# Kernel optimization log

Measured on AMD Instinct MI355X. Metric: run time of the kernel, lower is better.

## Reference

```python
import jax, jax.numpy as jnp
import numpy as np

B, L, H, C, A = 8, 4096, 512, 64, 512
NEG = -1000000000.0

def setup_inputs() -> dict:
    key = jax.random.key(0)
    ks = jax.random.split(key, 6)
    hidden_states = jax.random.normal(ks[0], (B, L, H), dtype=jnp.float32)
    critical_mask = jax.random.randint(ks[1], (B, L, 1), 0, 2).astype(bool)
    count_active_channels = jax.random.randint(ks[2], (B, L, 1), 0, 64).astype(jnp.int32)
    channel_activity = jax.random.normal(ks[3], (B, L, C), dtype=jnp.float32)
    proj_w = jax.random.normal(ks[4], (H, A), dtype=jnp.float32) * 0.02
    proj_b = jnp.zeros((A,), dtype=jnp.float32)
    score_w = jax.random.normal(ks[5], (A, 1), dtype=jnp.float32) * 0.02
    score_b = jnp.zeros((1,), dtype=jnp.float32)
    return {"hidden_states": hidden_states, "critical_mask": critical_mask,
            "count_active_channels": count_active_channels,
            "channel_activity": channel_activity,
            "proj_w": proj_w, "proj_b": proj_b,
            "score_w": score_w, "score_b": score_b}

def reference(hidden_states, critical_mask, count_active_channels, channel_activity,
              proj_w, proj_b, score_w, score_b):
    mask = critical_mask[..., 0].astype(bool)                       # (B,L)
    count_signal = count_active_channels[..., 0].astype(hidden_states.dtype)  # (B,L)
    activity = jnp.maximum(channel_activity.astype(hidden_states.dtype), 0.0)  # (B,L,C)
    # score(tanh(proj(h)))  -> (B,L)
    logits = (jnp.tanh(hidden_states @ proj_w + proj_b) @ score_w + score_b)[..., 0]
    logits = logits + jnp.log1p(jnp.maximum(count_signal, 0.0))
    channel_mask = activity > 0                                      # (B,L,C)
    # (B,C,L) masked logits with log1p activity bias
    channel_logits = logits[:, None, :] + jnp.log1p(jnp.swapaxes(activity, 1, 2))
    channel_logits = jnp.where(jnp.swapaxes(channel_mask, 1, 2), channel_logits, NEG)
    has_channel_any = channel_mask.any(axis=1)                       # (B,C)
    weights = jax.nn.softmax(channel_logits, axis=-1)                # (B,C,L)
    weights = jnp.where(has_channel_any[..., None], weights, 0.0)
    channel_contexts = jnp.einsum('bcl,blh->bch', weights, hidden_states)  # (B,C,H)
    fallback = jnp.broadcast_to(hidden_states[:, -1:, :], channel_contexts.shape)
    channel_contexts = jnp.where(has_channel_any[..., None], channel_contexts, fallback)
    mix = activity / jnp.maximum(activity.sum(axis=2, keepdims=True), 1.0)  # (B,L,C)
    expanded_context = jnp.einsum('blc,bch->blh', mix, channel_contexts)    # (B,L,H)
    max_count = jnp.maximum(count_signal.max(axis=1, keepdims=True), 1.0)
    density_gate = 1.0 + count_signal / max_count                    # (B,L)
    attended = jnp.where(mask[..., None], expanded_context * density_gate[..., None], hidden_states)
    return attended, weights
```

## Files before the change

kernel.cpp:

```cpp
#include <hip/hip_runtime.h>
#include <hip/hip_bf16.h>
#include <math.h>

#define NEGV (-1000000000.0f)
constexpr int Bb = 8, Ll = 4096, Hh = 512, Cc = 64, Aa = 512;

typedef float f32x4 __attribute__((ext_vector_type(4)));
typedef short s16x8 __attribute__((ext_vector_type(8)));

__device__ inline ushort f2bf(float f) {
  union { float f; uint u; } v; v.f = f;
  uint u = v.u;
  return (ushort)((u + 0x7FFFu + ((u >> 16) & 1u)) >> 16);
}

__device__ inline uint bfpack2(float x, float y) {
  __hip_bfloat162 h = __float22bfloat162_rn(make_float2(x, y));
  union { __hip_bfloat162 h; uint u; } v; v.h = h;
  return v.u;
}

__device__ __forceinline__ void gl16(const void* g, void* l) {
  __builtin_amdgcn_global_load_lds(
      reinterpret_cast<const __attribute__((address_space(1))) unsigned int*>(
          reinterpret_cast<uintptr_t>(g)),
      reinterpret_cast<__attribute__((address_space(3))) unsigned int*>(
          reinterpret_cast<uintptr_t>(l)),
      16, 0, 0);
}

__global__ void k_cvt(const float* __restrict__ hid, ushort* __restrict__ hidb) {
  size_t i = (size_t)blockIdx.x * 256 + threadIdx.x;
#pragma unroll
  for (int r = 0; r < 4; ++r, i += 524288) {
    const float4* p = (const float4*)(hid + i * 8);
    float4 x = p[0], y = p[1];
    uint4 u = {bfpack2(x.x, x.y), bfpack2(x.z, x.w),
               bfpack2(y.x, y.y), bfpack2(y.z, y.w)};
    *(uint4*)(hidb + i * 8) = u;
  }
}

__global__ void k_init(const int* __restrict__ cnt, const float* __restrict__ sb,
                       float* __restrict__ logits, int* __restrict__ cmax) {
  int i = blockIdx.x * 256 + threadIdx.x;
  int c = cnt[i];
  logits[i] = sb[0] + log1pf(fmaxf((float)c, 0.f));
  int m = c;
#pragma unroll
  for (int s = 32; s; s >>= 1) m = max(m, __shfl_xor(m, s));
  if ((threadIdx.x & 63) == 0) atomicMax(&cmax[i >> 12], m);
}

__global__ void kT_pw(const float* __restrict__ pw, ushort* __restrict__ pwT) {
  __shared__ ushort s[64][65];
  const int k0 = (blockIdx.x >> 3) * 64, a0 = (blockIdx.x & 7) * 64;
  const int t = threadIdx.x;
#pragma unroll
  for (int i = 0; i < 16; ++i) {
    int e = t + i * 256;
    int kk = e >> 6, aa = e & 63;
    s[aa][kk] = f2bf(pw[(size_t)(k0 + kk) * Aa + a0 + aa]);
  }
  __syncthreads();
#pragma unroll
  for (int i = 0; i < 16; ++i) {
    int e = t + i * 256;
    int aa = e >> 6, kk = e & 63;
    pwT[(size_t)(a0 + aa) * Hh + k0 + kk] = s[aa][kk];
  }
}

__global__ __launch_bounds__(256) void k0_gemm(
    const ushort* __restrict__ hidb, const ushort* __restrict__ pwT,
    const float* __restrict__ pb, const float* __restrict__ sw,
    float* __restrict__ logits) {
  __shared__ ushort smem[16384];
  const int bm = blockIdx.x, bn = blockIdx.y;
  const int tid = threadIdx.x;
  const int lane = tid & 63;
  const int w = tid >> 6;
  const int wm = w >> 1, wn = w & 1;
  const int lc = lane & 15, lq = lane >> 4;

  const int srow = tid >> 2;
  const int schunk = (tid & 3) * 8;
  const ushort* Ag = hidb + ((size_t)(bm * 128 + srow)) * Hh + schunk;
  const ushort* Bg = pwT + ((size_t)(bn * 128 + srow)) * Hh + schunk;
  const int wrow = 16 * w;

  f32x4 acc[4][4];
#pragma unroll
  for (int mi = 0; mi < 4; ++mi)
#pragma unroll
    for (int ni = 0; ni < 4; ++ni) acc[mi][ni] = (f32x4){0.f, 0.f, 0.f, 0.f};

  const int aoffc = (wm * 64 + lc) * 32 + lq * 8;
  const int boffc = (wn * 64 + lc) * 32 + lq * 8;

#define K0_STAGE(buf, kb)                                   \
  do {                                                      \
    const ushort* ag = Ag + (kb) * 32;                      \
    const ushort* bg = Bg + (kb) * 32;                      \
    ushort* la = smem + (buf) * 4096 + wrow * 32;           \
    ushort* lb = smem + 8192 + (buf) * 4096 + wrow * 32;    \
    gl16(ag, la);                                           \
    gl16(ag + 64 * Hh, la + 64 * 32);                       \
    gl16(bg, lb);                                           \
    gl16(bg + 64 * Hh, lb + 64 * 32);                       \
  } while (0)

  K0_STAGE(0, 0);
  __syncthreads();

  int buf = 0;
  for (int kb = 0; kb < 16; ++kb) {
    if (kb < 15) K0_STAGE(buf ^ 1, kb + 1);
    const ushort* Ab = smem + buf * 4096;
    const ushort* Bt = smem + 8192 + buf * 4096;
    s16x8 af[4], bfr[4];
#pragma unroll
    for (int mi = 0; mi < 4; ++mi)
      af[mi] = *(const s16x8*)(Ab + aoffc + mi * 512);
#pragma unroll
    for (int ni = 0; ni < 4; ++ni)
      bfr[ni] = *(const s16x8*)(Bt + boffc + ni * 512);
#pragma unroll
    for (int mi = 0; mi < 4; ++mi)
#pragma unroll
      for (int ni = 0; ni < 4; ++ni)
        acc[mi][ni] = __builtin_amdgcn_mfma_f32_16x16x32_bf16(
            af[mi], bfr[ni], acc[mi][ni], 0, 0, 0);
    __syncthreads();
    buf ^= 1;
  }
#undef K0_STAGE

  float pbv[4], swv[4];
#pragma unroll
  for (int ni = 0; ni < 4; ++ni) {
    int n = bn * 128 + wn * 64 + ni * 16 + lc;
    pbv[ni] = pb[n];
    swv[ni] = sw[n];
  }
#pragma unroll
  for (int mi = 0; mi < 4; ++mi) {
#pragma unroll
    for (int r = 0; r < 4; ++r) {
      float s = 0.f;
#pragma unroll
      for (int ni = 0; ni < 4; ++ni) {
        float x = acc[mi][ni][r] + pbv[ni];
        float e = __expf(2.f * x);
        float th = 1.f - 2.f / (e + 1.f);
        s = fmaf(th, swv[ni], s);
      }
      s += __shfl_xor(s, 1);
      s += __shfl_xor(s, 2);
      s += __shfl_xor(s, 4);
      s += __shfl_xor(s, 8);
      if (lc == 0) {
        int m = bm * 128 + wm * 64 + mi * 16 + lq * 4 + r;
        atomicAdd(&logits[m], s);
      }
    }
  }
}

__global__ void k2_transpose(const float* __restrict__ act,
                             float* __restrict__ actT,
                             float* __restrict__ dinv) {
  __shared__ float t64[64][65];
  const int b = blockIdx.x >> 6;
  const int l0 = (blockIdx.x & 63) * 64;
  const int tid = threadIdx.x;
#pragma unroll
  for (int i = 0; i < 16; ++i) {
    int e = tid + i * 256;
    int l = e >> 6, c = e & 63;
    float v = act[((size_t)(b * Ll + l0 + l)) * Cc + c];
    t64[l][c] = fmaxf(v, 0.f);
  }
  __syncthreads();
  if (tid < 64) {
    float s = 0.f;
#pragma unroll 8
    for (int c = 0; c < 64; ++c) s += t64[tid][c];
    dinv[b * Ll + l0 + tid] = 1.0f / fmaxf(s, 1.0f);
  }
#pragma unroll
  for (int i = 0; i < 16; ++i) {
    int e = tid + i * 256;
    int c = e >> 6, lq = e & 63;
    actT[((size_t)(b * Cc + c)) * Ll + l0 + lq] = t64[lq][c];
  }
}

__global__ void k3_softmax(const float* __restrict__ actT,
                           const float* __restrict__ logits,
                           float* __restrict__ wout,
                           ushort* __restrict__ wb16,
                           int* __restrict__ hasany) {
  __shared__ float rmax[4], rcnt[4], rsum[4];
  const int bid = blockIdx.x;
  const int b = bid >> 6;
  const int tid = threadIdx.x;
  const float* arow = actT + (size_t)bid * Ll;

  float xs[16];
  float lmax = NEGV, fcnt = 0.f;
#pragma unroll
  for (int i = 0; i < 16; ++i) {
    int l = tid + i * 256;
    float a = arow[l];
    float x;
    if (a > 0.f) {
      x = logits[b * Ll + l] + log1pf(a);
      fcnt += 1.f;
    } else {
      x = NEGV;
    }
    xs[i] = x;
    lmax = fmaxf(lmax, x);
  }
#pragma unroll
  for (int m = 32; m >= 1; m >>= 1) {
    lmax = fmaxf(lmax, __shfl_xor(lmax, m));
    fcnt += __shfl_xor(fcnt, m);
  }
  if ((tid & 63) == 0) { rmax[tid >> 6] = lmax; rcnt[tid >> 6] = fcnt; }
  __syncthreads();
  float m4 = fmaxf(fmaxf(rmax[0], rmax[1]), fmaxf(rmax[2], rmax[3]));
  float call = rcnt[0] + rcnt[1] + rcnt[2] + rcnt[3];

  float lsum = 0.f;
#pragma unroll
  for (int i = 0; i < 16; ++i) {
    float e = expf(xs[i] - m4);
    xs[i] = e;
    lsum += e;
  }
#pragma unroll
  for (int m = 32; m >= 1; m >>= 1) lsum += __shfl_xor(lsum, m);
  if ((tid & 63) == 0) rsum[tid >> 6] = lsum;
  __syncthreads();
  float s = rsum[0] + rsum[1] + rsum[2] + rsum[3];
  int any = call > 0.5f;
  float inv = any ? 1.0f / s : 0.f;
#pragma unroll
  for (int i = 0; i < 16; ++i) {
    float wv = xs[i] * inv;
    wout[(size_t)bid * Ll + tid + i * 256] = wv;
    wb16[(size_t)bid * Ll + tid + i * 256] = f2bf(wv);
  }
  if (tid == 0) hasany[bid] = any;
}

__global__ __launch_bounds__(256) void k5_mfma(
    const ushort* __restrict__ wb16, const ushort* __restrict__ hidb,
    float* __restrict__ pbuf) {
  const int b = blockIdx.x, nt = blockIdx.y, kz = blockIdx.z;
  const int tid = threadIdx.x;
  const int w = tid >> 6, lane = tid & 63;
  const int lc = lane & 15, lq = lane >> 4;
  const int h0 = nt * 128 + w * 32;

  f32x4 acc[4][2];
#pragma unroll
  for (int mi = 0; mi < 4; ++mi)
#pragma unroll
    for (int ni = 0; ni < 2; ++ni) acc[mi][ni] = (f32x4){0.f, 0.f, 0.f, 0.f};

  const ushort* Abase =
      wb16 + (size_t)b * Cc * Ll + (size_t)lc * Ll + kz * 256 + lq * 8;
  const ushort* Bbase =
      hidb + ((size_t)(b * Ll + kz * 256 + lq * 8)) * Hh + h0 + lc;

  for (int kb = 0; kb < 8; ++kb) {
    s16x8 af[4];
#pragma unroll
    for (int mi = 0; mi < 4; ++mi)
      af[mi] = *(const s16x8*)(Abase + (size_t)mi * 16 * Ll + kb * 32);
    s16x8 bfv[2];
#pragma unroll
    for (int ni = 0; ni < 2; ++ni) {
      const ushort* bp = Bbase + (size_t)kb * 32 * Hh + ni * 16;
      s16x8 t;
#pragma unroll
      for (int j = 0; j < 8; ++j) t[j] = (short)bp[(size_t)j * Hh];
      bfv[ni] = t;
    }
#pragma unroll
    for (int mi = 0; mi < 4; ++mi)
#pragma unroll
      for (int ni = 0; ni < 2; ++ni)
        acc[mi][ni] = __builtin_amdgcn_mfma_f32_16x16x32_bf16(
            af[mi], bfv[ni], acc[mi][ni], 0, 0, 0);
  }

  const size_t obase = ((size_t)(kz * Bb + b)) * Cc * Hh;
#pragma unroll
  for (int mi = 0; mi < 4; ++mi)
#pragma unroll
    for (int ni = 0; ni < 2; ++ni)
#pragma unroll
      for (int r = 0; r < 4; ++r)
        pbuf[obase + (size_t)(mi * 16 + lq * 4 + r) * Hh + h0 + ni * 16 + lc] =
            acc[mi][ni][r];
}

__global__ void k6_reduce(const float* __restrict__ pbuf,
                          const int* __restrict__ hasany,
                          const float* __restrict__ hid,
                          float* __restrict__ cctx) {
  int idx = blockIdx.x * 256 + threadIdx.x;
  float s = 0.f;
#pragma unroll
  for (int z = 0; z < 16; ++z) s += pbuf[(size_t)z * 262144 + idx];
  int bc = idx >> 9, b = idx >> 15, h = idx & 511;
  cctx[idx] = hasany[bc] ? s : hid[((size_t)(b * Ll + Ll - 1)) * Hh + h];
}

__global__ __launch_bounds__(256) void k7_out(
    const float* __restrict__ hid, const float* __restrict__ act,
    const float* __restrict__ dinv, const float* __restrict__ cctx,
    const int* __restrict__ mask, const int* __restrict__ cnt,
    const int* __restrict__ cmax, float* __restrict__ out) {
  __shared__ float cct[64][128];
  __shared__ float mixs[64][64];
  __shared__ float gateb[64];
  __shared__ int maskb[64];
  const int b = blockIdx.x;
  const int l0 = blockIdx.y * 64;
  const int h0 = blockIdx.z * 128;
  const int tid = threadIdx.x;
  const int w = tid >> 6;

  {
    const float* g = cctx + (size_t)(b * Cc + (tid >> 5)) * Hh + h0 + (tid & 31) * 4;
    float* lb = &cct[0][0] + (2 * w) * 128;
#pragma unroll
    for (int i = 0; i < 8; ++i)
      gl16(g + (size_t)(i * 8) * Hh, lb + i * 8 * 128);
  }
#pragma unroll
  for (int i = 0; i < 4; ++i) {
    int e = tid + i * 256;
    int t = e >> 4, c4 = (e & 15) * 4;
    float4 a4 = *(const float4*)(act + ((size_t)(b * Ll + l0 + t)) * Cc + c4);
    float dv = dinv[b * Ll + l0 + t];
    a4.x = fmaxf(a4.x, 0.f) * dv;
    a4.y = fmaxf(a4.y, 0.f) * dv;
    a4.z = fmaxf(a4.z, 0.f) * dv;
    a4.w = fmaxf(a4.w, 0.f) * dv;
    *(float4*)&mixs[t][c4] = a4;
  }
  if (tid < 64) {
    int l = l0 + tid;
    maskb[tid] = mask[b * Ll + l];
    gateb[tid] = 1.0f + (float)cnt[b * Ll + l] / fmaxf((float)cmax[b], 1.0f);
  }
  __syncthreads();

  const int hcol = (tid & 31) * 4;
  const int tok0 = (tid >> 5) * 8;

  f32x4 acc[8];
#pragma unroll
  for (int t = 0; t < 8; ++t) acc[t] = (f32x4){0.f, 0.f, 0.f, 0.f};

#pragma unroll 4
  for (int c0 = 0; c0 < 64; c0 += 4) {
    f32x4 cv0 = *(const f32x4*)&cct[c0 + 0][hcol];
    f32x4 cv1 = *(const f32x4*)&cct[c0 + 1][hcol];
    f32x4 cv2 = *(const f32x4*)&cct[c0 + 2][hcol];
    f32x4 cv3 = *(const f32x4*)&cct[c0 + 3][hcol];
#pragma unroll
    for (int t = 0; t < 8; ++t) {
      f32x4 mv = *(const f32x4*)&mixs[tok0 + t][c0];
      f32x4 a = acc[t];
      a = cv0 * mv.x + a;
      a = cv1 * mv.y + a;
      a = cv2 * mv.z + a;
      a = cv3 * mv.w + a;
      acc[t] = a;
    }
  }

#pragma unroll
  for (int t = 0; t < 8; ++t) {
    int tok = tok0 + t;
    size_t off = ((size_t)(b * Ll + l0 + tok)) * Hh + h0 + hcol;
    f32x4 o;
    if (maskb[tok]) {
      o = acc[t] * gateb[tok];
    } else {
      o = *(const f32x4*)(hid + off);
    }
    *(f32x4*)(out + off) = o;
  }
}

extern "C" void kernel_launch(void* const* d_in, const int* in_sizes, int n_in,
                              void* d_out, int out_size, void* d_ws,
                              size_t ws_size, hipStream_t stream) {
  const float* hid = (const float*)d_in[0];
  const int* mask = (const int*)d_in[1];
  const int* cnt = (const int*)d_in[2];
  const float* act = (const float*)d_in[3];
  const float* pw = (const float*)d_in[4];
  const float* pb = (const float*)d_in[5];
  const float* sw = (const float*)d_in[6];
  const float* sb = (const float*)d_in[7];

  float* out_att = (float*)d_out;
  float* out_w = out_att + (size_t)Bb * Ll * Hh;

  float* ws = (float*)d_ws;
  float* cctx = ws;
  int* cmaxi = (int*)(ws + 262144);
  float* logits = ws + 262152;
  float* actT = ws + 294920;
  float* dinv = ws + 2392072;
  int* hasany = (int*)(ws + 2424840);
  ushort* pwT = (ushort*)(ws + 2425352);
  ushort* wb16 = (ushort*)(ws + 2556424);
  float* pbuf = ws + 3605000;

  ushort* hidb = (ushort*)out_att;

  hipMemsetAsync(cmaxi, 0, 8 * sizeof(int), stream);

  k_cvt<<<2048, 256, 0, stream>>>(hid, hidb);
  k_init<<<128, 256, 0, stream>>>(cnt, sb, logits, cmaxi);
  kT_pw<<<64, 256, 0, stream>>>(pw, pwT);
  k0_gemm<<<dim3(256, 4), 256, 0, stream>>>(hidb, pwT, pb, sw, logits);
  k2_transpose<<<512, 256, 0, stream>>>(act, actT, dinv);
  k3_softmax<<<512, 256, 0, stream>>>(actT, logits, out_w, wb16, hasany);
  k5_mfma<<<dim3(8, 4, 16), 256, 0, stream>>>(wb16, hidb, pbuf);
  k6_reduce<<<1024, 256, 0, stream>>>(pbuf, hasany, hid, cctx);
  k7_out<<<dim3(8, 64, 4), 256, 0, stream>>>(hid, act, dinv, cctx, mask, cnt,
                                             cmaxi, out_att);
}
```

Measured before the change: 263.6 us.

## Produce transposed bf16 hidden copy so MFMA B-operand loads are vectorized

The bf16 conversion kernel now also writes a transposed (B,H,L) copy of the hidden states through an LDS tile, and the channel-context MFMA kernel reads its B fragments from that copy as contiguous 16-byte vectors. Previously each B fragment was gathered from eight scalar loads strided by H. This removes the strided 2-byte gathers in the GEMM. In exchange the conversion kernel does scalar 4-byte reads, an extra 2-byte-per-element write pass, and LDS transposes, and it uses more of the output buffer as scratch. The loop is also unrolled by two.

Result: no change. 265.0 us (+0.5%).

```diff
diff --git a/kernel.cpp b/kernel.cpp
--- a/kernel.cpp
+++ b/kernel.cpp
@@ -29,15 +29,29 @@
       16, 0, 0);
 }
 
-__global__ void k_cvt(const float* __restrict__ hid, ushort* __restrict__ hidb) {
-  size_t i = (size_t)blockIdx.x * 256 + threadIdx.x;
-#pragma unroll
-  for (int r = 0; r < 4; ++r, i += 524288) {
-    const float4* p = (const float4*)(hid + i * 8);
-    float4 x = p[0], y = p[1];
-    uint4 u = {bfpack2(x.x, x.y), bfpack2(x.z, x.w),
-               bfpack2(y.x, y.y), bfpack2(y.z, y.w)};
-    *(uint4*)(hidb + i * 8) = u;
+__global__ void k_cvtT(const float* __restrict__ hid, ushort* __restrict__ hidb,
+                       ushort* __restrict__ hidbT) {
+  __shared__ ushort s[64][65];
+  const int b = blockIdx.z;
+  const int l0 = blockIdx.x * 64;
+  const int h0 = blockIdx.y * 64;
+  const int tid = threadIdx.x;
+  const int lr = tid >> 6;
+  const int hc = tid & 63;
+#pragma unroll
+  for (int i = 0; i < 16; ++i) {
+    int l = lr + i * 4;
+    ushort v = f2bf(hid[((size_t)(b * Ll + l0 + l)) * Hh + h0 + hc]);
+    s[l][hc] = v;
+    hidb[((size_t)(b * Ll + l0 + l)) * Hh + h0 + hc] = v;
+  }
+  __syncthreads();
+#pragma unroll
+  for (int i = 0; i < 8; ++i) {
+    int e = tid + i * 256;
+    int ht = e >> 5, p = e & 31;
+    uint v = (uint)s[2 * p][ht] | ((uint)s[2 * p + 1][ht] << 16);
+    *(uint*)(hidbT + ((size_t)(b * Hh + h0 + ht)) * Ll + l0 + 2 * p) = v;
   }
 }
 
@@ -257,7 +271,7 @@
 }
 
 __global__ __launch_bounds__(256) void k5_mfma(
-    const ushort* __restrict__ wb16, const ushort* __restrict__ hidb,
+    const ushort* __restrict__ wb16, const ushort* __restrict__ hidbT,
     float* __restrict__ pbuf) {
   const int b = blockIdx.x, nt = blockIdx.y, kz = blockIdx.z;
   const int tid = threadIdx.x;
@@ -274,8 +288,9 @@
   const ushort* Abase =
       wb16 + (size_t)b * Cc * Ll + (size_t)lc * Ll + kz * 256 + lq * 8;
   const ushort* Bbase =
-      hidb + ((size_t)(b * Ll + kz * 256 + lq * 8)) * Hh + h0 + lc;
-
+      hidbT + ((size_t)(b * Hh + h0 + lc)) * Ll + kz * 256 + lq * 8;
+
+#pragma unroll 2
   for (int kb = 0; kb < 8; ++kb) {
     s16x8 af[4];
 #pragma unroll
@@ -283,13 +298,8 @@
       af[mi] = *(const s16x8*)(Abase + (size_t)mi * 16 * Ll + kb * 32);
     s16x8 bfv[2];
 #pragma unroll
-    for (int ni = 0; ni < 2; ++ni) {
-      const ushort* bp = Bbase + (size_t)kb * 32 * Hh + ni * 16;
-      s16x8 t;
-#pragma unroll
-      for (int j = 0; j < 8; ++j) t[j] = (short)bp[(size_t)j * Hh];
-      bfv[ni] = t;
-    }
+    for (int ni = 0; ni < 2; ++ni)
+      bfv[ni] = *(const s16x8*)(Bbase + (size_t)ni * 16 * Ll + kb * 32);
 #pragma unroll
     for (int mi = 0; mi < 4; ++mi)
 #pragma unroll
@@ -428,16 +438,17 @@
   float* pbuf = ws + 3605000;
 
   ushort* hidb = (ushort*)out_att;
+  ushort* hidbT = (ushort*)(out_att + 8388608);
 
   hipMemsetAsync(cmaxi, 0, 8 * sizeof(int), stream);
 
-  k_cvt<<<2048, 256, 0, stream>>>(hid, hidb);
+  k_cvtT<<<dim3(64, 8, 8), 256, 0, stream>>>(hid, hidb, hidbT);
   k_init<<<128, 256, 0, stream>>>(cnt, sb, logits, cmaxi);
   kT_pw<<<64, 256, 0, stream>>>(pw, pwT);
   k0_gemm<<<dim3(256, 4), 256, 0, stream>>>(hidb, pwT, pb, sw, logits);
   k2_transpose<<<512, 256, 0, stream>>>(act, actT, dinv);
   k3_softmax<<<512, 256, 0, stream>>>(actT, logits, out_w, wb16, hasany);
-  k5_mfma<<<dim3(8, 4, 16), 256, 0, stream>>>(wb16, hidb, pbuf);
+  k5_mfma<<<dim3(8, 4, 16), 256, 0, stream>>>(wb16, hidbT, pbuf);
   k6_reduce<<<1024, 256, 0, stream>>>(pbuf, hasany, hid, cctx);
   k7_out<<<dim3(8, 64, 4), 256, 0, stream>>>(hid, act, dinv, cctx, mask, cnt,
                                              cmaxi, out_att);
```
